# Kernel tuning notes

Hardware: AMD Instinct MI355X
Metric: run time of the kernel (lower is better)

## Reference

```python
import jax, jax.numpy as jnp
import numpy as np

B, S, E, H = 2, 2048, 1024, 16
D = E // H  # head_dim = 64
SCALE = D ** -0.5


def setup_inputs() -> dict:
    key = jax.random.key(0)
    ks = jax.random.split(key, 5)
    std = E ** -0.5
    return {
        "x": jax.random.normal(ks[0], (B, S, E), dtype=jnp.float32),
        "wq": jax.random.normal(ks[1], (E, E), dtype=jnp.float32) * std,
        "wk": jax.random.normal(ks[2], (E, E), dtype=jnp.float32) * std,
        "wv": jax.random.normal(ks[3], (E, E), dtype=jnp.float32) * std,
        "wo": jax.random.normal(ks[4], (E, E), dtype=jnp.float32) * std,
    }


def reference(x, wq, wk, wv, wo):
    b, s, e = x.shape
    # nn.Linear(bias=False): y = x @ W.T; then split heads -> [B,H,S,D]
    def heads(w):
        return jnp.einsum('bse,fe->bsf', x, w).reshape(b, s, H, D).transpose(0, 2, 1, 3)
    q, k, v = heads(wq), heads(wk), heads(wv)
    attn = jnp.einsum('bhqd,bhkd->bhqk', q, k) * SCALE  # [B,H,S,S]
    attn = jax.nn.softmax(attn, axis=-1)
    out = jnp.einsum('bhqk,bhkd->bhqd', attn, v)        # [B,H,S,D]
    out = out.transpose(0, 2, 1, 3).reshape(b, s, e)
    return jnp.einsum('bse,fe->bsf', out, wo)
```

## Files before the change

kernel.cpp:

```cpp
#include <hip/hip_runtime.h>
#include <stdint.h>

typedef unsigned short ushort_t;
typedef __bf16 bfx8 __attribute__((ext_vector_type(8), may_alias));
typedef unsigned short usx8 __attribute__((ext_vector_type(8), may_alias));
typedef float f32x4 __attribute__((ext_vector_type(4)));
typedef float f32x4m __attribute__((ext_vector_type(4), may_alias));

#define BB 2
#define SS 2048
#define EE 1024
#define HH 16
#define DD 64
#define MM (BB * SS)
#define XN ((size_t)MM * EE)
#define WN ((size_t)EE * EE)
#define PS_STRIDE 76
#define QSCALE 0.18033688011112042f

__device__ __forceinline__ unsigned short f2bf(float f) {
  unsigned int u = __builtin_bit_cast(unsigned int, f);
  u += 0x7fffu + ((u >> 16) & 1u);
  return (unsigned short)(u >> 16);
}

__device__ __forceinline__ usx8 cvt8(const float* p) {
  f32x4m a = *(const f32x4m*)p;
  f32x4m b = *(const f32x4m*)(p + 4);
  usx8 r;
  r[0] = f2bf(a[0]); r[1] = f2bf(a[1]); r[2] = f2bf(a[2]); r[3] = f2bf(a[3]);
  r[4] = f2bf(b[0]); r[5] = f2bf(b[1]); r[6] = f2bf(b[2]); r[7] = f2bf(b[3]);
  return r;
}

__device__ __forceinline__ void stc(ushort_t* p, float v) { *p = f2bf(v); }
__device__ __forceinline__ void stc(float* p, float v) { *p = v; }

__device__ __forceinline__ void gl_lds16(const ushort_t* g, ushort_t* l) {
  __builtin_amdgcn_global_load_lds(
      (const __attribute__((address_space(1))) unsigned int*)g,
      (__attribute__((address_space(3))) unsigned int*)l, 16, 0, 0);
}

__global__ __launch_bounds__(256)
void cvt_qkv(const float* __restrict__ x, const float* __restrict__ wq,
             const float* __restrict__ wk, const float* __restrict__ wv,
             ushort_t* __restrict__ dst) {
  size_t i8 = ((size_t)blockIdx.x * 256 + threadIdx.x) * 8;
  const float* s;
  size_t off;
  if (i8 < XN)               { s = x;  off = i8; }
  else if (i8 < XN + WN)     { s = wq; off = i8 - XN; }
  else if (i8 < XN + 2 * WN) { s = wk; off = i8 - XN - WN; }
  else                       { s = wv; off = i8 - XN - 2 * WN; }
  *(usx8*)(dst + i8) = cvt8(s + off);
}

__global__ __launch_bounds__(256)
void cvt_one(const float* __restrict__ s, ushort_t* __restrict__ dst) {
  size_t i8 = ((size_t)blockIdx.x * 256 + threadIdx.x) * 8;
  *(usx8*)(dst + i8) = cvt8(s + i8);
}

__global__ __launch_bounds__(256)
void gemm_qkv(const ushort_t* __restrict__ xb,
              const ushort_t* __restrict__ wqb, const ushort_t* __restrict__ wkb,
              const ushort_t* __restrict__ wvb,
              ushort_t* __restrict__ Qb, ushort_t* __restrict__ Kb,
              ushort_t* __restrict__ Vtb) {
  __shared__ ushort_t As[128 * 32];
  __shared__ ushort_t Bs[128 * 32];

  const int bid = blockIdx.x;
  const ushort_t *A, *W;
  ushort_t* C;
  int bx, by, N;
  float scale = 1.0f;
  if (bid < 512) {
    int t = bid & 255;
    bx = t & 7;  by = t >> 3;
    A = xb;  N = EE;
    if (bid < 256) { W = wqb; C = Qb; scale = QSCALE; }
    else           { W = wkb; C = Kb; }
  } else {
    int t = bid - 512;
    bx = t & 31; by = t >> 5;
    A = wvb; W = xb; C = Vtb; N = MM;
  }
  const int K = EE;

  const int tid = threadIdx.x;
  const int lane = tid & 63;
  const int w = tid >> 6;
  const int l15 = lane & 15, l16 = lane >> 4;
  const int m0 = by * 128;
  const int n0 = bx * 128;
  const int wr = w >> 1, wc = w & 1;

  f32x4 acc[4][4];
#pragma unroll
  for (int i = 0; i < 4; ++i)
#pragma unroll
    for (int j = 0; j < 4; ++j)
#pragma unroll
      for (int r = 0; r < 4; ++r) acc[i][j][r] = 0.0f;

  for (int k0 = 0; k0 < K; k0 += 32) {
#pragma unroll
    for (int q = 0; q < 2; ++q) {
      int c = w * 128 + q * 64 + lane;
      int row = c >> 2, col = c & 3;
      gl_lds16(A + (size_t)(m0 + row) * K + k0 + col * 8,
               As + (size_t)(w * 128 + q * 64) * 8);
      gl_lds16(W + (size_t)(n0 + row) * K + k0 + col * 8,
               Bs + (size_t)(w * 128 + q * 64) * 8);
    }
    __syncthreads();

    bfx8 af[4], bfr[4];
#pragma unroll
    for (int i = 0; i < 4; ++i) {
      int mr = wr * 64 + i * 16 + l15;
      af[i] = *(const bfx8*)(As + mr * 32 + l16 * 8);
      int nr = wc * 64 + i * 16 + l15;
      bfr[i] = *(const bfx8*)(Bs + nr * 32 + l16 * 8);
    }
#pragma unroll
    for (int i = 0; i < 4; ++i)
#pragma unroll
      for (int j = 0; j < 4; ++j)
        acc[i][j] = __builtin_amdgcn_mfma_f32_16x16x32_bf16(af[i], bfr[j],
                                                            acc[i][j], 0, 0, 0);
    __syncthreads();
  }

#pragma unroll
  for (int i = 0; i < 4; ++i) {
    int mr = m0 + wr * 64 + i * 16 + l16 * 4;
#pragma unroll
    for (int j = 0; j < 4; ++j) {
      int nc = n0 + wc * 64 + j * 16 + l15;
#pragma unroll
      for (int r = 0; r < 4; ++r)
        C[(size_t)(mr + r) * N + nc] = f2bf(acc[i][j][r] * scale);
    }
  }
}

__global__ __launch_bounds__(256)
void gemm_o(const ushort_t* __restrict__ A, const ushort_t* __restrict__ W,
            float* __restrict__ C, int M, int N, int K) {
  __shared__ ushort_t As[128 * 32];
  __shared__ ushort_t Bs[128 * 32];

  const int tid = threadIdx.x;
  const int lane = tid & 63;
  const int w = tid >> 6;
  const int l15 = lane & 15, l16 = lane >> 4;
  const int m0 = blockIdx.y * 128;
  const int n0 = blockIdx.x * 128;
  const int wr = w >> 1, wc = w & 1;

  f32x4 acc[4][4];
#pragma unroll
  for (int i = 0; i < 4; ++i)
#pragma unroll
    for (int j = 0; j < 4; ++j)
#pragma unroll
      for (int r = 0; r < 4; ++r) acc[i][j][r] = 0.0f;

  for (int k0 = 0; k0 < K; k0 += 32) {
#pragma unroll
    for (int q = 0; q < 2; ++q) {
      int c = w * 128 + q * 64 + lane;
      int row = c >> 2, col = c & 3;
      gl_lds16(A + (size_t)(m0 + row) * K + k0 + col * 8,
               As + (size_t)(w * 128 + q * 64) * 8);
      gl_lds16(W + (size_t)(n0 + row) * K + k0 + col * 8,
               Bs + (size_t)(w * 128 + q * 64) * 8);
    }
    __syncthreads();

    bfx8 af[4], bfr[4];
#pragma unroll
    for (int i = 0; i < 4; ++i) {
      int mr = wr * 64 + i * 16 + l15;
      af[i] = *(const bfx8*)(As + mr * 32 + l16 * 8);
      int nr = wc * 64 + i * 16 + l15;
      bfr[i] = *(const bfx8*)(Bs + nr * 32 + l16 * 8);
    }
#pragma unroll
    for (int i = 0; i < 4; ++i)
#pragma unroll
      for (int j = 0; j < 4; ++j)
        acc[i][j] = __builtin_amdgcn_mfma_f32_16x16x32_bf16(af[i], bfr[j],
                                                            acc[i][j], 0, 0, 0);
    __syncthreads();
  }

#pragma unroll
  for (int i = 0; i < 4; ++i) {
    int mr = m0 + wr * 64 + i * 16 + l16 * 4;
#pragma unroll
    for (int j = 0; j < 4; ++j) {
      int nc = n0 + wc * 64 + j * 16 + l15;
#pragma unroll
      for (int r = 0; r < 4; ++r)
        C[(size_t)(mr + r) * N + nc] = acc[i][j][r];
    }
  }
}

__global__ __launch_bounds__(256)
void attn_fwd(const ushort_t* Q, const ushort_t* __restrict__ Kg,
              const ushort_t* __restrict__ Vt_g, ushort_t* AO) {
  __shared__ ushort_t Ks[64 * 72];
  __shared__ ushort_t Vs[64 * 72];
  __shared__ __bf16 Ps[4][16 * PS_STRIDE];

  const int tid = threadIdx.x;
  const int lane = tid & 63;
  const int w = tid >> 6;
  const int l15 = lane & 15, l16 = lane >> 4;
  const int qt = blockIdx.x, h = blockIdx.y, b = blockIdx.z;
  const int q0 = qt * 64 + w * 16;

  bfx8 aq[2];
#pragma unroll
  for (int kk = 0; kk < 2; ++kk)
    aq[kk] = *(const bfx8*)(Q + ((size_t)(b * SS + q0 + l15)) * EE + h * DD +
                            kk * 32 + l16 * 8);

  f32x4 o[4];
  float lsum[4];
#pragma unroll
  for (int c = 0; c < 4; ++c)
#pragma unroll
    for (int r = 0; r < 4; ++r) o[c][r] = 0.0f;
#pragma unroll
  for (int r = 0; r < 4; ++r) lsum[r] = 0.0f;

  for (int kt = 0; kt < SS; kt += 64) {
    usx8 kreg[2], vreg[2];
    int cr[2], cc[2];
#pragma unroll
    for (int i = 0; i < 2; ++i) {
      int c = tid + i * 256;
      cr[i] = c >> 3;
      cc[i] = c & 7;
      kreg[i] = *(const usx8*)(Kg + ((size_t)(b * SS + kt + cr[i])) * EE +
                               h * DD + cc[i] * 8);
      vreg[i] = *(const usx8*)(Vt_g + ((size_t)(h * DD + cr[i])) * MM +
                               b * SS + kt + cc[i] * 8);
    }
    __syncthreads();
#pragma unroll
    for (int i = 0; i < 2; ++i) {
      *(usx8*)(Ks + cr[i] * 72 + cc[i] * 8) = kreg[i];
      *(usx8*)(Vs + cr[i] * 72 + cc[i] * 8) = vreg[i];
    }
    __syncthreads();

    f32x4 sf[4];
#pragma unroll
    for (int j = 0; j < 4; ++j) {
      f32x4 t;
#pragma unroll
      for (int r = 0; r < 4; ++r) t[r] = 0.0f;
#pragma unroll
      for (int kk = 0; kk < 2; ++kk) {
        int n = j * 16 + l15;
        bfx8 bk = *(const bfx8*)(Ks + n * 72 + (kk * 4 + l16) * 8);
        t = __builtin_amdgcn_mfma_f32_16x16x32_bf16(aq[kk], bk, t, 0, 0, 0);
      }
      sf[j] = t;
    }

#pragma unroll
    for (int j = 0; j < 4; ++j)
#pragma unroll
      for (int r = 0; r < 4; ++r) {
        float p = __builtin_exp2f(sf[j][r]);
        sf[j][r] = p;
        lsum[r] += p;
      }

    asm volatile("" ::: "memory");
#pragma unroll
    for (int j = 0; j < 4; ++j)
#pragma unroll
      for (int r = 0; r < 4; ++r)
        Ps[w][(l16 * 4 + r) * PS_STRIDE + j * 16 + l15] = (__bf16)sf[j][r];
    asm volatile("" ::: "memory");

    bfx8 ap[2];
#pragma unroll
    for (int kkk = 0; kkk < 2; ++kkk)
      ap[kkk] = *(const bfx8*)(&Ps[w][l15 * PS_STRIDE + kkk * 32 + l16 * 8]);
#pragma unroll
    for (int c = 0; c < 4; ++c)
#pragma unroll
      for (int kkk = 0; kkk < 2; ++kkk) {
        bfx8 bv = *(const bfx8*)(Vs + (c * 16 + l15) * 72 + kkk * 32 + l16 * 8);
        o[c] = __builtin_amdgcn_mfma_f32_16x16x32_bf16(ap[kkk], bv, o[c], 0, 0, 0);
      }
  }

#pragma unroll
  for (int r = 0; r < 4; ++r) {
#pragma unroll
    for (int d = 1; d < 16; d <<= 1) lsum[r] += __shfl_xor(lsum[r], d);
    lsum[r] = 1.0f / lsum[r];
  }
#pragma unroll
  for (int c = 0; c < 4; ++c)
#pragma unroll
    for (int r = 0; r < 4; ++r)
      AO[((size_t)(b * SS + q0 + l16 * 4 + r)) * EE + h * DD + c * 16 + l15] =
          f2bf(o[c][r] * lsum[r]);
}

extern "C" void kernel_launch(void* const* d_in, const int* in_sizes, int n_in,
                              void* d_out, int out_size, void* d_ws, size_t ws_size,
                              hipStream_t stream) {
  const float* x  = (const float*)d_in[0];
  const float* wq = (const float*)d_in[1];
  const float* wk = (const float*)d_in[2];
  const float* wv = (const float*)d_in[3];
  const float* wo = (const float*)d_in[4];
  float* out = (float*)d_out;

  ushort_t* Qb  = (ushort_t*)d_ws;
  ushort_t* Kb  = Qb + XN;
  ushort_t* Vtb = Kb + XN;
  ushort_t* Ab  = Qb;
  ushort_t* S    = (ushort_t*)d_out;
  ushort_t* xb   = S;
  ushort_t* wqb  = S + XN;
  ushort_t* wkb  = S + XN + WN;
  ushort_t* wvb  = S + XN + 2 * WN;
  ushort_t* wob  = Kb;

  dim3 blk(256);
  cvt_qkv<<<dim3((unsigned)((XN + 3 * WN) / (256 * 8))), blk, 0, stream>>>(
      x, wq, wk, wv, S);
  gemm_qkv<<<dim3(768), blk, 0, stream>>>(xb, wqb, wkb, wvb, Qb, Kb, Vtb);
  attn_fwd<<<dim3(SS / 64, HH, BB), blk, 0, stream>>>(Qb, Kb, Vtb, Ab);
  cvt_one<<<dim3((unsigned)(WN / (256 * 8))), blk, 0, stream>>>(wo, wob);
  gemm_o<<<dim3(EE / 128, MM / 128), blk, 0, stream>>>(
      Ab, wob, out, MM, EE, EE);
}
```

Before: 219.6 us.

## Rewrite attention with 32x32 MFMA, transposed scores, and register-only P via permlane swap

```diff
diff --git a/kernel.cpp b/kernel.cpp
--- a/kernel.cpp
+++ b/kernel.cpp
@@ -3,9 +3,13 @@
 
 typedef unsigned short ushort_t;
 typedef __bf16 bfx8 __attribute__((ext_vector_type(8), may_alias));
+typedef __bf16 bfx2 __attribute__((ext_vector_type(2), may_alias));
 typedef unsigned short usx8 __attribute__((ext_vector_type(8), may_alias));
+typedef unsigned int uix2 __attribute__((ext_vector_type(2), may_alias));
+typedef unsigned int uix4 __attribute__((ext_vector_type(4), may_alias));
 typedef float f32x4 __attribute__((ext_vector_type(4)));
 typedef float f32x4m __attribute__((ext_vector_type(4), may_alias));
+typedef float f32x16 __attribute__((ext_vector_type(16)));
 
 #define BB 2
 #define SS 2048
@@ -15,7 +19,6 @@
 #define MM (BB * SS)
 #define XN ((size_t)MM * EE)
 #define WN ((size_t)EE * EE)
-#define PS_STRIDE 76
 #define QSCALE 0.18033688011112042f
 
 __device__ __forceinline__ unsigned short f2bf(float f) {
@@ -33,8 +36,12 @@
   return r;
 }
 
-__device__ __forceinline__ void stc(ushort_t* p, float v) { *p = f2bf(v); }
-__device__ __forceinline__ void stc(float* p, float v) { *p = v; }
+__device__ __forceinline__ unsigned int pk2(float lo, float hi) {
+  bfx2 t;
+  t[0] = (__bf16)lo;
+  t[1] = (__bf16)hi;
+  return __builtin_bit_cast(unsigned int, t);
+}
 
 __device__ __forceinline__ void gl_lds16(const ushort_t* g, ushort_t* l) {
   __builtin_amdgcn_global_load_lds(
@@ -211,113 +218,131 @@
   }
 }
 
-__global__ __launch_bounds__(256)
+__global__ __launch_bounds__(128)
 void attn_fwd(const ushort_t* Q, const ushort_t* __restrict__ Kg,
               const ushort_t* __restrict__ Vt_g, ushort_t* AO) {
   __shared__ ushort_t Ks[64 * 72];
   __shared__ ushort_t Vs[64 * 72];
-  __shared__ __bf16 Ps[4][16 * PS_STRIDE];
 
   const int tid = threadIdx.x;
   const int lane = tid & 63;
   const int w = tid >> 6;
-  const int l15 = lane & 15, l16 = lane >> 4;
+  const int l31 = lane & 31, hi = lane >> 5;
   const int qt = blockIdx.x, h = blockIdx.y, b = blockIdx.z;
-  const int q0 = qt * 64 + w * 16;
-
-  bfx8 aq[2];
-#pragma unroll
-  for (int kk = 0; kk < 2; ++kk)
-    aq[kk] = *(const bfx8*)(Q + ((size_t)(b * SS + q0 + l15)) * EE + h * DD +
-                            kk * 32 + l16 * 8);
-
-  f32x4 o[4];
-  float lsum[4];
-#pragma unroll
-  for (int c = 0; c < 4; ++c)
-#pragma unroll
-    for (int r = 0; r < 4; ++r) o[c][r] = 0.0f;
-#pragma unroll
-  for (int r = 0; r < 4; ++r) lsum[r] = 0.0f;
+  const int q0 = qt * 64 + w * 32;
+
+  bfx8 bq[4];
+#pragma unroll
+  for (int t = 0; t < 4; ++t)
+    bq[t] = *(const bfx8*)(Q + (size_t)(b * SS + q0 + l31) * EE + h * DD +
+                           t * 16 + hi * 8);
+
+  f32x16 o0, o1;
+#pragma unroll
+  for (int r = 0; r < 16; ++r) { o0[r] = 0.0f; o1[r] = 0.0f; }
+  float lsum = 0.0f;
+
+  int cr[4], cc[4];
+#pragma unroll
+  for (int i = 0; i < 4; ++i) {
+    int c = tid + i * 128;
+    cr[i] = c >> 3;
+    cc[i] = c & 7;
+  }
+  const ushort_t* kbase = Kg + (size_t)b * SS * EE + h * DD;
+  const ushort_t* vbase = Vt_g + (size_t)h * DD * MM + (size_t)b * SS;
+
+  usx8 kreg[4], vreg[4];
+#pragma unroll
+  for (int i = 0; i < 4; ++i) {
+    kreg[i] = *(const usx8*)(kbase + (size_t)cr[i] * EE + cc[i] * 8);
+    vreg[i] = *(const usx8*)(vbase + (size_t)cr[i] * MM + cc[i] * 8);
+  }
 
   for (int kt = 0; kt < SS; kt += 64) {
-    usx8 kreg[2], vreg[2];
-    int cr[2], cc[2];
-#pragma unroll
-    for (int i = 0; i < 2; ++i) {
-      int c = tid + i * 256;
-      cr[i] = c >> 3;
-      cc[i] = c & 7;
-      kreg[i] = *(const usx8*)(Kg + ((size_t)(b * SS + kt + cr[i])) * EE +
-                               h * DD + cc[i] * 8);
-      vreg[i] = *(const usx8*)(Vt_g + ((size_t)(h * DD + cr[i])) * MM +
-                               b * SS + kt + cc[i] * 8);
-    }
-    __syncthreads();
-#pragma unroll
-    for (int i = 0; i < 2; ++i) {
+    __syncthreads();
+#pragma unroll
+    for (int i = 0; i < 4; ++i) {
       *(usx8*)(Ks + cr[i] * 72 + cc[i] * 8) = kreg[i];
       *(usx8*)(Vs + cr[i] * 72 + cc[i] * 8) = vreg[i];
     }
     __syncthreads();
-
-    f32x4 sf[4];
-#pragma unroll
-    for (int j = 0; j < 4; ++j) {
-      f32x4 t;
-#pragma unroll
-      for (int r = 0; r < 4; ++r) t[r] = 0.0f;
-#pragma unroll
-      for (int kk = 0; kk < 2; ++kk) {
-        int n = j * 16 + l15;
-        bfx8 bk = *(const bfx8*)(Ks + n * 72 + (kk * 4 + l16) * 8);
-        t = __builtin_amdgcn_mfma_f32_16x16x32_bf16(aq[kk], bk, t, 0, 0, 0);
+    if (kt + 64 < SS) {
+#pragma unroll
+      for (int i = 0; i < 4; ++i) {
+        kreg[i] =
+            *(const usx8*)(kbase + (size_t)(kt + 64 + cr[i]) * EE + cc[i] * 8);
+        vreg[i] =
+            *(const usx8*)(vbase + (size_t)cr[i] * MM + kt + 64 + cc[i] * 8);
       }
-      sf[j] = t;
-    }
-
-#pragma unroll
-    for (int j = 0; j < 4; ++j)
-#pragma unroll
-      for (int r = 0; r < 4; ++r) {
-        float p = __builtin_exp2f(sf[j][r]);
-        sf[j][r] = p;
-        lsum[r] += p;
-      }
-
-    asm volatile("" ::: "memory");
-#pragma unroll
-    for (int j = 0; j < 4; ++j)
-#pragma unroll
-      for (int r = 0; r < 4; ++r)
-        Ps[w][(l16 * 4 + r) * PS_STRIDE + j * 16 + l15] = (__bf16)sf[j][r];
-    asm volatile("" ::: "memory");
-
-    bfx8 ap[2];
-#pragma unroll
-    for (int kkk = 0; kkk < 2; ++kkk)
-      ap[kkk] = *(const bfx8*)(&Ps[w][l15 * PS_STRIDE + kkk * 32 + l16 * 8]);
-#pragma unroll
-    for (int c = 0; c < 4; ++c)
-#pragma unroll
-      for (int kkk = 0; kkk < 2; ++kkk) {
-        bfx8 bv = *(const bfx8*)(Vs + (c * 16 + l15) * 72 + kkk * 32 + l16 * 8);
-        o[c] = __builtin_amdgcn_mfma_f32_16x16x32_bf16(ap[kkk], bv, o[c], 0, 0, 0);
-      }
-  }
-
-#pragma unroll
-  for (int r = 0; r < 4; ++r) {
-#pragma unroll
-    for (int d = 1; d < 16; d <<= 1) lsum[r] += __shfl_xor(lsum[r], d);
-    lsum[r] = 1.0f / lsum[r];
-  }
-#pragma unroll
-  for (int c = 0; c < 4; ++c)
-#pragma unroll
-    for (int r = 0; r < 4; ++r)
-      AO[((size_t)(b * SS + q0 + l16 * 4 + r)) * EE + h * DD + c * 16 + l15] =
-          f2bf(o[c][r] * lsum[r]);
+    }
+
+    f32x16 pa, pb;
+#pragma unroll
+    for (int r = 0; r < 16; ++r) { pa[r] = 0.0f; pb[r] = 0.0f; }
+#pragma unroll
+    for (int t = 0; t < 4; ++t) {
+      bfx8 ak0 = *(const bfx8*)(Ks + l31 * 72 + t * 16 + hi * 8);
+      bfx8 ak1 = *(const bfx8*)(Ks + (32 + l31) * 72 + t * 16 + hi * 8);
+      pa = __builtin_amdgcn_mfma_f32_32x32x16_bf16(ak0, bq[t], pa, 0, 0, 0);
+      pb = __builtin_amdgcn_mfma_f32_32x32x16_bf16(ak1, bq[t], pb, 0, 0, 0);
+    }
+
+#pragma unroll
+    for (int r = 0; r < 16; ++r) {
+      pa[r] = __builtin_exp2f(pa[r]);
+      pb[r] = __builtin_exp2f(pb[r]);
+      lsum += pa[r] + pb[r];
+    }
+
+    unsigned int dwA[8], dwB[8];
+#pragma unroll
+    for (int s = 0; s < 8; ++s) {
+      dwA[s] = pk2(pa[2 * s], pa[2 * s + 1]);
+      dwB[s] = pk2(pb[2 * s], pb[2 * s + 1]);
+    }
+    bfx8 fd[4];
+#pragma unroll
+    for (int g = 0; g < 2; ++g) {
+      auto sA = __builtin_amdgcn_permlane32_swap(dwA[4 * g + 0], dwA[4 * g + 2],
+                                                 false, false);
+      auto sB = __builtin_amdgcn_permlane32_swap(dwA[4 * g + 1], dwA[4 * g + 3],
+                                                 false, false);
+      uix4 f;
+      f[0] = sA[0]; f[1] = sB[0]; f[2] = sA[1]; f[3] = sB[1];
+      fd[g] = __builtin_bit_cast(bfx8, f);
+      auto tA = __builtin_amdgcn_permlane32_swap(dwB[4 * g + 0], dwB[4 * g + 2],
+                                                 false, false);
+      auto tB = __builtin_amdgcn_permlane32_swap(dwB[4 * g + 1], dwB[4 * g + 3],
+                                                 false, false);
+      uix4 f2;
+      f2[0] = tA[0]; f2[1] = tB[0]; f2[2] = tA[1]; f2[3] = tB[1];
+      fd[2 + g] = __builtin_bit_cast(bfx8, f2);
+    }
+
+#pragma unroll
+    for (int kk = 0; kk < 4; ++kk) {
+      bfx8 av0 = *(const bfx8*)(Vs + l31 * 72 + kk * 16 + hi * 8);
+      bfx8 av1 = *(const bfx8*)(Vs + (32 + l31) * 72 + kk * 16 + hi * 8);
+      o0 = __builtin_amdgcn_mfma_f32_32x32x16_bf16(av0, fd[kk], o0, 0, 0, 0);
+      o1 = __builtin_amdgcn_mfma_f32_32x32x16_bf16(av1, fd[kk], o1, 0, 0, 0);
+    }
+  }
+
+  lsum += __shfl_xor(lsum, 32);
+  float inv = 1.0f / lsum;
+
+  ushort_t* orow = AO + (size_t)(b * SS + q0 + l31) * EE + h * DD;
+#pragma unroll
+  for (int g = 0; g < 4; ++g) {
+    uix2 s0, s1;
+    s0[0] = pk2(o0[4 * g + 0] * inv, o0[4 * g + 1] * inv);
+    s0[1] = pk2(o0[4 * g + 2] * inv, o0[4 * g + 3] * inv);
+    *(uix2*)(orow + 8 * g + 4 * hi) = s0;
+    s1[0] = pk2(o1[4 * g + 0] * inv, o1[4 * g + 1] * inv);
+    s1[1] = pk2(o1[4 * g + 2] * inv, o1[4 * g + 3] * inv);
+    *(uix2*)(orow + 32 + 8 * g + 4 * hi) = s1;
+  }
 }
 
 extern "C" void kernel_launch(void* const* d_in, const int* in_sizes, int n_in,
@@ -345,7 +370,7 @@
   cvt_qkv<<<dim3((unsigned)((XN + 3 * WN) / (256 * 8))), blk, 0, stream>>>(
       x, wq, wk, wv, S);
   gemm_qkv<<<dim3(768), blk, 0, stream>>>(xb, wqb, wkb, wvb, Qb, Kb, Vtb);
-  attn_fwd<<<dim3(SS / 64, HH, BB), blk, 0, stream>>>(Qb, Kb, Vtb, Ab);
+  attn_fwd<<<dim3(SS / 64, HH, BB), dim3(128), 0, stream>>>(Qb, Kb, Vtb, Ab);
   cvt_one<<<dim3((unsigned)(WN / (256 * 8))), blk, 0, stream>>>(wo, wob);
   gemm_o<<<dim3(EE / 128, MM / 128), blk, 0, stream>>>(
       Ab, wob, out, MM, EE, EE);
```

After: 212.4 us. -3.3%, faster.
